# Kernel optimization log

Hardware: AMD Instinct MI355X
Metric: run time of the kernel (lower is better)

The kernel has to match this reference:

```python
import jax, jax.numpy as jnp
import numpy as np

HW = 24       # image_size // patch_size
HEAD = 16     # vision num_attention_heads
B, T, C, H = 8, 8, 1024, 4096


def _sincos_1d(d, pos):
    omega = np.arange(d // 2, dtype=np.float32) / (d / 2.0)
    omega = 1.0 / 10000 ** omega
    out = np.einsum('m,d->md', pos.reshape(-1).astype(np.float32), omega)
    return np.concatenate([np.sin(out), np.cos(out)], axis=1)


def _pos_embed_3d(embed_dim, grid_size, t_size):
    ds = embed_dim // 4 * 3
    dt = embed_dim // 4
    gh = np.arange(grid_size, dtype=np.float32)
    grid = np.stack(np.meshgrid(gh, gh), axis=0).reshape(2, -1)  # (w, h) order as in source
    spatial = np.concatenate([_sincos_1d(ds // 2, grid[0]), _sincos_1d(ds // 2, grid[1])], axis=1)  # [g*g, ds]
    temporal = _sincos_1d(dt, np.arange(t_size, dtype=np.float32))  # [t, dt]
    spatial = np.repeat(spatial[np.newaxis], t_size, axis=0)                 # [t, g*g, ds]
    temporal = np.repeat(temporal[:, np.newaxis], grid_size ** 2, axis=1)    # [t, g*g, dt]
    emb = np.concatenate([temporal, spatial], axis=-1)
    return emb.reshape(1, t_size * grid_size ** 2, embed_dim).astype(np.float32)


def setup_inputs() -> dict:
    key = jax.random.key(0)
    k1, k2, k3 = jax.random.split(key, 3)
    x = jax.random.normal(k1, (B, T * HW * HW, C), dtype=jnp.float32)
    W1 = jax.random.normal(k2, (C, H), dtype=jnp.float32) * 0.02
    b1 = jnp.zeros((H,), jnp.float32)
    W2 = jax.random.normal(k3, (H, H), dtype=jnp.float32) * 0.02
    b2 = jnp.zeros((H,), jnp.float32)
    pos_embed = jnp.asarray(_pos_embed_3d(C, HW, T))
    return {"x": x, "pos_embed": pos_embed, "W1": W1, "b1": b1, "W2": W2, "b2": b2,
            "local_num_frames": T}


def _merge(x, unm_idx, src_idx, dst_idx):
    # ToMe merge: gather unmatched src tokens, scatter-add matched src into dst.
    src, dst = x[:, ::2], x[:, 1::2]
    unm = jnp.take_along_axis(src, unm_idx[:, :, None], axis=1)   # [b, t1-r, c]
    sel = jnp.take_along_axis(src, src_idx[:, :, None], axis=1)   # [b, r, c]
    dst = jax.vmap(lambda d, i, s: d.at[i].add(s))(dst, dst_idx, sel)
    return jnp.concatenate([unm, dst], axis=1)


def _merge_tokens(x, target, head):
    b, p, c = x.shape
    # static merge schedule (same logic as torch merge_tokens)
    rs, tmp = [], p
    while tmp != target:
        if tmp - target <= tmp // 2:
            rs.append(tmp - target)
            break
        rs.append(tmp // 2)
        tmp -= tmp // 2
    dim = c // head
    size = jnp.ones((b, p, 1), x.dtype)
    for r in rs:
        bb, pp, _ = x.shape
        # metric/index computation is under no_grad in the original
        metric = jax.lax.stop_gradient(x).reshape(bb, pp, head, dim).mean(2)
        metric = metric / jnp.linalg.norm(metric, axis=-1, keepdims=True)
        a_m, b_m = metric[:, ::2], metric[:, 1::2]
        scores = jnp.einsum('bic,bjc->bij', a_m, b_m)  # [b, ta, tb]
        node_max = scores.max(-1)
        node_idx = scores.argmax(-1)
        edge_idx = jnp.argsort(-node_max, axis=-1)      # descending
        unm_idx, src_idx = edge_idx[:, r:], edge_idx[:, :r]
        dst_idx = jnp.take_along_axis(node_idx, src_idx, axis=1)
        # weighted-average merge (merge_wavg)
        x = _merge(x * size, unm_idx, src_idx, dst_idx)
        size = _merge(size, unm_idx, src_idx, dst_idx)
        x = x / size
    return x


def reference(x, pos_embed, W1, b1, W2, b2, local_num_frames):
    x = x + pos_embed.astype(x.dtype)
    x = _merge_tokens(x, local_num_frames * 16, HEAD)
    h = jax.nn.gelu(x @ W1 + b1, approximate=False)  # nn.GELU() is exact erf gelu
    return h @ W2 + b2
```

## Files before the change

kernel.cpp:

```cpp
#include <hip/hip_runtime.h>
#include <hip/hip_bf16.h>
#include <math.h>
#include <stdint.h>

typedef unsigned short u16;
typedef __attribute__((ext_vector_type(8))) short short8;
typedef __attribute__((ext_vector_type(4))) float floatx4;

#define NB 8
#define P0 4608
#define C0 1024
#define H0 4096

__global__ void detect_mode_kernel(const uint32_t* __restrict__ pe_words, int* __restrict__ mode) {
  *mode = (pe_words[64] != 0u) ? 1 : 0;
}

__device__ __forceinline__ float load_in(const void* p, size_t idx, int mode) {
  if (mode) return __bfloat162float(((const __hip_bfloat16*)p)[idx]);
  return ((const float*)p)[idx];
}

__device__ __forceinline__ float4 load4(const void* p, size_t idx, int mode) {
  float4 r;
  if (mode) {
    ushort4 u = *(const ushort4*)((const u16*)p + idx);
    r.x = __bfloat162float(*(__hip_bfloat16*)&u.x);
    r.y = __bfloat162float(*(__hip_bfloat16*)&u.y);
    r.z = __bfloat162float(*(__hip_bfloat16*)&u.z);
    r.w = __bfloat162float(*(__hip_bfloat16*)&u.w);
  } else {
    r = *(const float4*)((const float*)p + idx);
  }
  return r;
}

__device__ __forceinline__ void write_hilo(u16* __restrict__ m2, size_t tok, int lane, float v) {
  __hip_bfloat16 hi = __float2bfloat16(v);
  float hif = __bfloat162float(hi);
  __hip_bfloat16 lo = __float2bfloat16(v - hif);
  m2[tok * 128 + lane] = *(u16*)&hi;
  m2[tok * 128 + 64 + lane] = *(u16*)&lo;
}

__global__ void metric_in_kernel(const void* __restrict__ x, const void* __restrict__ pos,
                                 const int* __restrict__ mode, u16* __restrict__ m2) {
  int tok = blockIdx.x * 4 + (threadIdx.x >> 6);
  int lane = threadIdx.x & 63;
  if (tok >= NB * P0) return;
  int b = tok / P0, t = tok - b * P0;
  int md = *mode;
  size_t xbase = ((size_t)b * P0 + t) * C0 + lane;
  size_t pbase = (size_t)t * C0 + lane;
  float s = 0.f;
#pragma unroll
  for (int h = 0; h < 16; ++h)
    s += load_in(x, xbase + h * 64, md) + load_in(pos, pbase + h * 64, md);
  s *= (1.f / 16.f);
  float sq = s * s;
#pragma unroll
  for (int off = 1; off < 64; off <<= 1) sq += __shfl_xor(sq, off, 64);
  write_hilo(m2, (size_t)tok, lane, s / sqrtf(sq));
}

__global__ void metric_f32_kernel(const float* __restrict__ x, u16* __restrict__ m2, int p) {
  int tok = blockIdx.x * 4 + (threadIdx.x >> 6);
  int lane = threadIdx.x & 63;
  if (tok >= NB * p) return;
  const float* xr = x + (size_t)tok * C0 + lane;
  float s = 0.f;
#pragma unroll
  for (int h = 0; h < 16; ++h) s += xr[h * 64];
  s *= (1.f / 16.f);
  float sq = s * s;
#pragma unroll
  for (int off = 1; off < 64; off <<= 1) sq += __shfl_xor(sq, off, 64);
  write_hilo(m2, (size_t)tok, lane, s / sqrtf(sq));
}

__global__ __launch_bounds__(256) void score_mfma_kernel(const u16* __restrict__ M2,
                                                         int p, int p2, int jT2,
                                                         float* __restrict__ pm,
                                                         int* __restrict__ pi) {
  const int bi = blockIdx.x, ii = blockIdx.y, b = blockIdx.z;
  const int t = threadIdx.x, w = t >> 6, L = t & 63;
  const int wr = w >> 1, wc = w & 1;
  const int fr = L & 15, fo = (L >> 4) * 8;
  const u16* Mb = M2 + (size_t)b * p * 128;

  floatx4 acc[4][4];
#pragma unroll
  for (int mt = 0; mt < 4; ++mt)
#pragma unroll
    for (int nt = 0; nt < 4; ++nt) acc[mt][nt] = (floatx4){0.f, 0.f, 0.f, 0.f};

  const u16* arp[4];
  const u16* brp[4];
#pragma unroll
  for (int mt = 0; mt < 4; ++mt) {
    int i = ii * 128 + wr * 64 + mt * 16 + fr;
    int ta = 2 * i;
    if (ta > p - 2) ta = p - 2;
    arp[mt] = Mb + (size_t)ta * 128 + fo;
    int j = bi * 128 + wc * 64 + mt * 16 + fr;
    int tb = 2 * j + 1;
    if (tb > p - 1) tb = p - 1;
    brp[mt] = Mb + (size_t)tb * 128 + fo;
  }

#pragma unroll
  for (int ks = 0; ks < 2; ++ks) {
    short8 ah[4], al[4], bh[4], bl[4];
#pragma unroll
    for (int mt = 0; mt < 4; ++mt) {
      ah[mt] = *(const short8*)(arp[mt] + ks * 32);
      al[mt] = *(const short8*)(arp[mt] + ks * 32 + 64);
      bh[mt] = *(const short8*)(brp[mt] + ks * 32);
      bl[mt] = *(const short8*)(brp[mt] + ks * 32 + 64);
    }
#pragma unroll
    for (int mt = 0; mt < 4; ++mt)
#pragma unroll
      for (int nt = 0; nt < 4; ++nt) {
        acc[mt][nt] = __builtin_amdgcn_mfma_f32_16x16x32_bf16(ah[mt], bh[nt], acc[mt][nt], 0, 0, 0);
        acc[mt][nt] = __builtin_amdgcn_mfma_f32_16x16x32_bf16(ah[mt], bl[nt], acc[mt][nt], 0, 0, 0);
        acc[mt][nt] = __builtin_amdgcn_mfma_f32_16x16x32_bf16(al[mt], bh[nt], acc[mt][nt], 0, 0, 0);
        acc[mt][nt] = __builtin_amdgcn_mfma_f32_16x16x32_bf16(al[mt], bl[nt], acc[mt][nt], 0, 0, 0);
      }
  }

  const int gi4 = (L >> 4) * 4;
#pragma unroll
  for (int mt = 0; mt < 4; ++mt) {
#pragma unroll
    for (int reg = 0; reg < 4; ++reg) {
      int i = ii * 128 + wr * 64 + mt * 16 + gi4 + reg;
      float bm = -INFINITY;
      int bj = 0x7fffffff;
#pragma unroll
      for (int nt = 0; nt < 4; ++nt) {
        int j = bi * 128 + wc * 64 + nt * 16 + fr;
        float v = acc[mt][nt][reg];
        if (j < p2 && v > bm) { bm = v; bj = j; }
      }
#pragma unroll
      for (int mk = 1; mk < 16; mk <<= 1) {
        float om = __shfl_xor(bm, mk, 64);
        int oj = __shfl_xor(bj, mk, 64);
        if (om > bm || (om == bm && oj < bj)) { bm = om; bj = oj; }
      }
      if (fr == 0 && i < p2) {
        size_t o = ((size_t)b * 2304 + i) * jT2 + bi * 2 + wc;
        pm[o] = bm;
        pi[o] = bj;
      }
    }
  }
}

__global__ void argmax_combine_kernel(const float* __restrict__ pm, const int* __restrict__ pi,
                                      int p2, int jT, float* __restrict__ nmax,
                                      int* __restrict__ nidx, int* __restrict__ head,
                                      int* __restrict__ nxt) {
  int g = blockIdx.x * 256 + threadIdx.x;
  if (g >= NB * p2) return;
  int b = g / p2, i = g - b * p2;
  const float* r = pm + ((size_t)b * 2304 + i) * jT;
  const int* ri = pi + ((size_t)b * 2304 + i) * jT;
  float best = r[0];
  int bidx = ri[0];
  for (int k = 1; k < jT; ++k) {
    if (r[k] > best || (r[k] == best && ri[k] < bidx)) { best = r[k]; bidx = ri[k]; }
  }
  nmax[g] = best;
  nidx[g] = bidx;
  int d = bidx;
  if ((unsigned)d >= (unsigned)p2) d = 0;
  nxt[g] = atomicExch(&head[(size_t)b * p2 + d], i);
}

__global__ void init_heads_kernel(int* __restrict__ h, int n) {
  int g = blockIdx.x * 256 + threadIdx.x;
  if (g < n) h[g] = -1;
}

__global__ __launch_bounds__(256) void merge_gather_in(const void* __restrict__ x,
                                                       const void* __restrict__ pos,
                                                       const int* __restrict__ mode,
                                                       const int* __restrict__ head,
                                                       const int* __restrict__ nxt,
                                                       float* __restrict__ xo,
                                                       float* __restrict__ so, int p2) {
  int tj = blockIdx.x;
  int b = tj / p2, j = tj - b * p2;
  int c = threadIdx.x * 4;
  int md = *mode;
  __shared__ int sl[64];
  __shared__ int s_n, s_cur;
  size_t xb = ((size_t)b * P0 + 2 * j + 1) * C0 + c;
  size_t pb = (size_t)(2 * j + 1) * C0 + c;
  float4 xa = load4(x, xb, md), pa = load4(pos, pb, md);
  float4 acc = {xa.x + pa.x, xa.y + pa.y, xa.z + pa.z, xa.w + pa.w};
  float cnt = 1.f;
  if (threadIdx.x == 0) s_cur = head[tj];
  __syncthreads();
  int cur = s_cur;
  while (cur != -1) {
    if (threadIdx.x == 0) {
      int n = 0, cc = cur;
      while (cc != -1 && n < 64) {
        sl[n++] = cc;
        cc = nxt[(size_t)b * p2 + cc];
      }
      s_n = n;
      s_cur = cc;
    }
    __syncthreads();
    int n = s_n;
    cur = s_cur;
    for (int k = 0; k < n; ++k) {
      int i = sl[k];
      size_t exb = ((size_t)b * P0 + 2 * i) * C0 + c;
      size_t epb = (size_t)(2 * i) * C0 + c;
      float4 ea = load4(x, exb, md), ep = load4(pos, epb, md);
      acc.x += ea.x + ep.x;
      acc.y += ea.y + ep.y;
      acc.z += ea.z + ep.z;
      acc.w += ea.w + ep.w;
      cnt += 1.f;
    }
    __syncthreads();
  }
  float inv = 1.f / cnt;
  float4 o = {acc.x * inv, acc.y * inv, acc.z * inv, acc.w * inv};
  *(float4*)(xo + (size_t)tj * C0 + c) = o;
  if (threadIdx.x == 0) so[tj] = cnt;
}

__global__ __launch_bounds__(256) void merge_gather_f(const float* __restrict__ xi,
                                                      const float* __restrict__ si,
                                                      const int* __restrict__ head,
                                                      const int* __restrict__ nxt,
                                                      float* __restrict__ xo,
                                                      float* __restrict__ so, int p, int p2) {
  int tj = blockIdx.x;
  int b = tj / p2, j = tj - b * p2;
  int c = threadIdx.x * 4;
  __shared__ int sl[64];
  __shared__ int s_n, s_cur;
  float sz = si[(size_t)b * p + 2 * j + 1];
  float4 v = *(const float4*)(xi + ((size_t)b * p + 2 * j + 1) * C0 + c);
  float4 acc = {v.x * sz, v.y * sz, v.z * sz, v.w * sz};
  float ssum = sz;
  if (threadIdx.x == 0) s_cur = head[tj];
  __syncthreads();
  int cur = s_cur;
  while (cur != -1) {
    if (threadIdx.x == 0) {
      int n = 0, cc = cur;
      while (cc != -1 && n < 64) {
        sl[n++] = cc;
        cc = nxt[(size_t)b * p2 + cc];
      }
      s_n = n;
      s_cur = cc;
    }
    __syncthreads();
    int n = s_n;
    cur = s_cur;
    for (int k = 0; k < n; ++k) {
      int i = sl[k];
      float szi = si[(size_t)b * p + 2 * i];
      float4 e = *(const float4*)(xi + ((size_t)b * p + 2 * i) * C0 + c);
      acc.x += e.x * szi;
      acc.y += e.y * szi;
      acc.z += e.z * szi;
      acc.w += e.w * szi;
      ssum += szi;
    }
    __syncthreads();
  }
  float inv = 1.f / ssum;
  float4 o = {acc.x * inv, acc.y * inv, acc.z * inv, acc.w * inv};
  *(float4*)(xo + (size_t)tj * C0 + c) = o;
  if (threadIdx.x == 0) so[tj] = ssum;
}

__global__ void rank_kernel(const float* __restrict__ nmax, const int* __restrict__ nidx,
                            int* __restrict__ unm_map, int* __restrict__ src_ord,
                            int* __restrict__ src_dst) {
  int b = blockIdx.x;
  int i = threadIdx.x;
  __shared__ float v[72];
  __shared__ int nx[72];
  if (i < 72) { v[i] = nmax[b * 72 + i]; nx[i] = nidx[b * 72 + i]; }
  __syncthreads();
  if (i < 72) {
    float vi = v[i];
    int rank = 0;
    for (int k = 0; k < 72; ++k) {
      float vk = v[k];
      rank += (vk > vi) || (vk == vi && k < i);
    }
    if (rank < 16) {
      int d = nx[i];
      if ((unsigned)d >= 72u) d = 0;
      src_ord[b * 16 + rank] = i;
      src_dst[b * 16 + rank] = d;
    } else {
      unm_map[b * 56 + (rank - 16)] = i;
    }
  }
}

__global__ void final_init(const float* __restrict__ x5, const float* __restrict__ s5,
                           const int* __restrict__ unm_map, float* __restrict__ xf,
                           float* __restrict__ sf) {
  int bt = blockIdx.x;
  int b = bt >> 7, tk = bt & 127;
  int c = threadIdx.x * 4;
  float4 o;
  float szo;
  if (tk < 56) {
    int se = unm_map[b * 56 + tk];
    if ((unsigned)se >= 72u) se = 0;
    o = *(const float4*)(x5 + ((size_t)b * 144 + 2 * se) * C0 + c);
    szo = 1.f;
  } else {
    int j = tk - 56;
    float sz = s5[b * 144 + 2 * j + 1];
    float4 v = *(const float4*)(x5 + ((size_t)b * 144 + 2 * j + 1) * C0 + c);
    o.x = v.x * sz; o.y = v.y * sz; o.z = v.z * sz; o.w = v.w * sz;
    szo = sz;
  }
  *(float4*)(xf + (size_t)bt * C0 + c) = o;
  if (threadIdx.x == 0) sf[bt] = szo;
}

__global__ void final_scatter(const float* __restrict__ x5, const float* __restrict__ s5,
                              const int* __restrict__ src_ord, const int* __restrict__ src_dst,
                              float* __restrict__ xf, float* __restrict__ sf) {
  int bk = blockIdx.x;
  int b = bk >> 4, k = bk & 15;
  int c = threadIdx.x * 4;
  int st = src_ord[b * 16 + k], dst = src_dst[b * 16 + k];
  if ((unsigned)st >= 72u) st = 0;
  if ((unsigned)dst >= 72u) dst = 0;
  float sz = s5[b * 144 + 2 * st];
  float4 v = *(const float4*)(x5 + ((size_t)b * 144 + 2 * st) * C0 + c);
  float* out = xf + ((size_t)(b * 128 + 56 + dst)) * C0 + c;
  atomicAdd(out + 0, v.x * sz);
  atomicAdd(out + 1, v.y * sz);
  atomicAdd(out + 2, v.z * sz);
  atomicAdd(out + 3, v.w * sz);
  if (threadIdx.x == 0) atomicAdd(sf + b * 128 + 56 + dst, sz);
}

__global__ void final_div_cvt(const float* __restrict__ xf, const float* __restrict__ sf,
                              __hip_bfloat16* __restrict__ xb) {
  int bt = blockIdx.x;
  int c = threadIdx.x * 4;
  float sz = sf[bt];
  float4 v = *(const float4*)(xf + (size_t)bt * C0 + c);
  __hip_bfloat16* o = xb + (size_t)bt * C0 + c;
  o[0] = __float2bfloat16(v.x / sz);
  o[1] = __float2bfloat16(v.y / sz);
  o[2] = __float2bfloat16(v.z / sz);
  o[3] = __float2bfloat16(v.w / sz);
}

__global__ void transpose_in(const void* __restrict__ in, const int* __restrict__ mode,
                             u16* __restrict__ out, int K, int N) {
  __shared__ u16 tile[64][65];
  int n0 = blockIdx.x * 64, k0 = blockIdx.y * 64;
  int t = threadIdx.x;
  int md = *mode;
  int r = t >> 4, c4 = (t & 15) * 4;
#pragma unroll
  for (int pass = 0; pass < 4; ++pass) {
    int row = r + pass * 16;
#pragma unroll
    for (int e = 0; e < 4; ++e) {
      float v = load_in(in, (size_t)(k0 + row) * N + n0 + c4 + e, md);
      __hip_bfloat16 bv = __float2bfloat16(v);
      tile[row][c4 + e] = *(u16*)&bv;
    }
  }
  __syncthreads();
#pragma unroll
  for (int pass = 0; pass < 4; ++pass) {
    int row = r + pass * 16;
    ushort4 o;
    o.x = tile[c4][row]; o.y = tile[c4 + 1][row]; o.z = tile[c4 + 2][row]; o.w = tile[c4 + 3][row];
    *(ushort4*)(out + (size_t)(n0 + row) * K + k0 + c4) = o;
  }
}

#define GL2LDS(gp, lp)                                                                   \
  __builtin_amdgcn_global_load_lds((const __attribute__((address_space(1))) uint32_t*)(gp), \
                                   (__attribute__((address_space(3))) uint32_t*)(lp), 16, 0, 0)

__global__ __launch_bounds__(256, 2) void gemm_bt(const u16* __restrict__ A,
                                                  const u16* __restrict__ BT,
                                                  const void* __restrict__ bias,
                                                  const int* __restrict__ mode,
                                                  void* __restrict__ C, int M, int N,
                                                  int K, int act, int out_sel) {
  __shared__ __align__(16) u16 As[2 * 64 * 64];
  __shared__ __align__(16) u16 Bs[2 * 128 * 64];
  const int t = threadIdx.x, w = t >> 6, L = t & 63;
  const int m0 = blockIdx.y * 64, n0 = blockIdx.x * 128;
  const int wr = w >> 1, wc = w & 1;
  const int md = *mode;
  const int fr = L & 15, fq = (L >> 4) * 8;
  floatx4 acc[2][4];
#pragma unroll
  for (int a = 0; a < 2; ++a)
#pragma unroll
    for (int bb = 0; bb < 4; ++bb) acc[a][bb] = (floatx4){0.f, 0.f, 0.f, 0.f};

  auto stage = [&](int buf, int kk) {
#pragma unroll
    for (int q = 0; q < 2; ++q) {
      int g = q * 256 + t;
      int row = g >> 3, colg = (g & 7) ^ (row & 7);
      GL2LDS(A + (size_t)(m0 + row) * K + kk + colg * 8, As + buf * 4096 + g * 8);
    }
#pragma unroll
    for (int q = 0; q < 4; ++q) {
      int g = q * 256 + t;
      int row = g >> 3, colg = (g & 7) ^ (row & 7);
      GL2LDS(BT + (size_t)(n0 + row) * K + kk + colg * 8, Bs + buf * 8192 + g * 8);
    }
  };

  stage(0, 0);
  const int NT = K >> 6;
  int cur = 0;
  for (int it = 0; it < NT; ++it) {
    if (it + 1 < NT) {
      stage(cur ^ 1, (it + 1) << 6);
      asm volatile("s_waitcnt vmcnt(6)" ::: "memory");
    } else {
      asm volatile("s_waitcnt vmcnt(0)" ::: "memory");
    }
    __builtin_amdgcn_s_barrier();
    const u16* Ab = As + cur * 4096;
    const u16* Bb = Bs + cur * 8192;
    __builtin_amdgcn_s_setprio(1);
#pragma unroll
    for (int kh = 0; kh < 2; ++kh) {
      short8 af[2], bfr[4];
#pragma unroll
      for (int mt = 0; mt < 2; ++mt) {
        int ra = wr * 32 + mt * 16 + fr;
        int cg = (kh * 4 + (L >> 4)) ^ (ra & 7);
        af[mt] = *(const short8*)(Ab + ra * 64 + cg * 8);
      }
#pragma unroll
      for (int nt = 0; nt < 4; ++nt) {
        int rb = wc * 64 + nt * 16 + fr;
        int cg = (kh * 4 + (L >> 4)) ^ (rb & 7);
        bfr[nt] = *(const short8*)(Bb + rb * 64 + cg * 8);
      }
#pragma unroll
      for (int mt = 0; mt < 2; ++mt)
#pragma unroll
        for (int nt = 0; nt < 4; ++nt)
          acc[mt][nt] =
              __builtin_amdgcn_mfma_f32_16x16x32_bf16(af[mt], bfr[nt], acc[mt][nt], 0, 0, 0);
    }
    __builtin_amdgcn_s_setprio(0);
    __builtin_amdgcn_s_barrier();
    cur ^= 1;
  }
  const int gi4 = (L >> 4) * 4;
#pragma unroll
  for (int mt = 0; mt < 2; ++mt)
#pragma unroll
    for (int nt = 0; nt < 4; ++nt) {
      int n = n0 + wc * 64 + nt * 16 + fr;
      float bz = load_in(bias, n, md);
#pragma unroll
      for (int rr = 0; rr < 4; ++rr) {
        int m = m0 + wr * 32 + mt * 16 + gi4 + rr;
        float v = acc[mt][nt][rr] + bz;
        if (act) v = 0.5f * v * (1.f + erff(v * 0.70710678118654752f));
        size_t idx = (size_t)m * N + n;
        if (out_sel == 0 || md) {
          __hip_bfloat16 bv = __float2bfloat16(v);
          ((u16*)C)[idx] = *(u16*)&bv;
        } else {
          ((float*)C)[idx] = v;
        }
      }
    }
}

extern "C" void kernel_launch(void* const* d_in, const int* in_sizes, int n_in, void* d_out,
                              int out_size, void* d_ws, size_t ws_size, hipStream_t stream) {
  const void* x = d_in[0];
  const void* pe = d_in[1];
  const void* W1 = d_in[2];
  const void* b1 = d_in[3];
  const void* W2 = d_in[4];
  const void* b2 = d_in[5];

  char* base = (char*)d_ws;
  size_t off = 0;
  auto alloc = [&](size_t bytes) -> void* {
    void* p = base + off;
    off += (bytes + 255) & ~(size_t)255;
    return p;
  };
  int* mode = (int*)alloc(256);
  u16* m2 = (u16*)alloc((size_t)NB * 4608 * 128 * 2);
  float* pm = (float*)alloc((size_t)NB * 2304 * 36 * 4);
  int* pi = (int*)alloc((size_t)NB * 2304 * 36 * 4);
  float* nmax = (float*)alloc((size_t)NB * 2304 * 4);
  int* nidx = (int*)alloc((size_t)NB * 2304 * 4);
  float* bufA = (float*)alloc((size_t)NB * 2304 * C0 * 4);
  float* bufB = (float*)alloc((size_t)NB * 1152 * C0 * 4);
  float* s1 = (float*)alloc((size_t)NB * 2304 * 4);
  float* s2 = (float*)alloc((size_t)NB * 1152 * 4);
  float* s3 = (float*)alloc((size_t)NB * 576 * 4);
  float* s4 = (float*)alloc((size_t)NB * 288 * 4);
  float* s5 = (float*)alloc((size_t)NB * 144 * 4);
  float* sf = (float*)alloc((size_t)NB * 128 * 4);
  int* unm_map = (int*)alloc((size_t)NB * 56 * 4);
  int* src_ord = (int*)alloc((size_t)NB * 16 * 4);
  int* src_dst = (int*)alloc((size_t)NB * 16 * 4);
  u16* xfb = (u16*)alloc((size_t)NB * 128 * C0 * 2);
  u16* hbuf = (u16*)alloc((size_t)1024 * H0 * 2);
  u16* w1t = (u16*)alloc((size_t)H0 * C0 * 2);
  u16* w2t = (u16*)alloc((size_t)H0 * H0 * 2);
  int* heads = (int*)alloc((size_t)NB * 4536 * 4);
  int* nxt = (int*)alloc((size_t)NB * 2304 * 4);
  if (off > ws_size) return;

  int* h_it[6];
  h_it[0] = heads;
  h_it[1] = h_it[0] + NB * 2304;
  h_it[2] = h_it[1] + NB * 1152;
  h_it[3] = h_it[2] + NB * 576;
  h_it[4] = h_it[3] + NB * 288;
  h_it[5] = h_it[4] + NB * 144;

  float* x1 = bufA;
  float* x2 = bufB;
  float* x3 = bufA;
  float* x4 = bufB;
  float* x5 = bufA;
  float* xf = bufB;

  detect_mode_kernel<<<1, 1, 0, stream>>>((const uint32_t*)pe, mode);
  init_heads_kernel<<<(NB * 4536 + 255) / 256, 256, 0, stream>>>(heads, NB * 4536);

  transpose_in<<<dim3(4096 / 64, 1024 / 64), 256, 0, stream>>>(W1, mode, w1t, 1024, 4096);
  transpose_in<<<dim3(4096 / 64, 4096 / 64), 256, 0, stream>>>(W2, mode, w2t, 4096, 4096);

  metric_in_kernel<<<NB * P0 / 4, 256, 0, stream>>>(x, pe, mode, m2);
  score_mfma_kernel<<<dim3(18, 18, NB), 256, 0, stream>>>(m2, 4608, 2304, 36, pm, pi);
  argmax_combine_kernel<<<(NB * 2304 + 255) / 256, 256, 0, stream>>>(pm, pi, 2304, 36, nmax,
                                                                     nidx, h_it[0], nxt);
  merge_gather_in<<<NB * 2304, 256, 0, stream>>>(x, pe, mode, h_it[0], nxt, x1, s1, 2304);

  float* xs_in[4] = {x1, x2, x3, x4};
  float* ss_in[4] = {s1, s2, s3, s4};
  float* xs_out[4] = {x2, x3, x4, x5};
  float* ss_out[4] = {s2, s3, s4, s5};
  int ps[5] = {2304, 1152, 576, 288, 144};
  for (int it = 0; it < 4; ++it) {
    int p = ps[it], p2 = ps[it + 1];
    int iT = (p2 + 127) / 128, jT = (p2 + 127) / 128;
    metric_f32_kernel<<<NB * p / 4, 256, 0, stream>>>(xs_in[it], m2, p);
    score_mfma_kernel<<<dim3(jT, iT, NB), 256, 0, stream>>>(m2, p, p2, 2 * jT, pm, pi);
    argmax_combine_kernel<<<(NB * p2 + 255) / 256, 256, 0, stream>>>(pm, pi, p2, 2 * jT, nmax,
                                                                     nidx, h_it[it + 1], nxt);
    merge_gather_f<<<NB * p2, 256, 0, stream>>>(xs_in[it], ss_in[it], h_it[it + 1], nxt,
                                                xs_out[it], ss_out[it], p, p2);
  }

  metric_f32_kernel<<<NB * 144 / 4, 256, 0, stream>>>(x5, m2, 144);
  score_mfma_kernel<<<dim3(1, 1, NB), 256, 0, stream>>>(m2, 144, 72, 2, pm, pi);
  argmax_combine_kernel<<<(NB * 72 + 255) / 256, 256, 0, stream>>>(pm, pi, 72, 2, nmax, nidx,
                                                                   h_it[5], nxt);
  rank_kernel<<<NB, 128, 0, stream>>>(nmax, nidx, unm_map, src_ord, src_dst);
  final_init<<<NB * 128, 256, 0, stream>>>(x5, s5, unm_map, xf, sf);
  final_scatter<<<NB * 16, 256, 0, stream>>>(x5, s5, src_ord, src_dst, xf, sf);
  final_div_cvt<<<NB * 128, 256, 0, stream>>>(xf, sf, (__hip_bfloat16*)xfb);

  gemm_bt<<<dim3(4096 / 128, 1024 / 64), 256, 0, stream>>>(xfb, w1t, b1, mode, hbuf, 1024, 4096,
                                                           1024, 1, 0);
  gemm_bt<<<dim3(4096 / 128, 1024 / 64), 256, 0, stream>>>(hbuf, w2t, b2, mode, d_out, 1024,
                                                           4096, 4096, 0, 1);
}
```

Before: 782.1 us.

## Fuse metric computation into merge-gather kernels and vectorize transpose loads

Each merge-gather kernel now computes the head-averaged, normalized metric for its output token from the values it just produced, writing the hi/lo bf16 metric directly. This removes the separate metric_f32 kernel launches and their re-read of the merged activations. The input metric kernel and the weight transpose kernel also specialize on the dtype mode, and the transpose now uses vector loads. A risk is that merge-gather rewrites m2 while the score kernel of the same stage reads it; stream ordering should make this safe since score runs earlier.

After: 754.6 us. -3.5%, faster.

```diff
diff --git a/kernel.cpp b/kernel.cpp
--- a/kernel.cpp
+++ b/kernel.cpp
@@ -53,24 +53,18 @@
   size_t xbase = ((size_t)b * P0 + t) * C0 + lane;
   size_t pbase = (size_t)t * C0 + lane;
   float s = 0.f;
-#pragma unroll
-  for (int h = 0; h < 16; ++h)
-    s += load_in(x, xbase + h * 64, md) + load_in(pos, pbase + h * 64, md);
-  s *= (1.f / 16.f);
-  float sq = s * s;
-#pragma unroll
-  for (int off = 1; off < 64; off <<= 1) sq += __shfl_xor(sq, off, 64);
-  write_hilo(m2, (size_t)tok, lane, s / sqrtf(sq));
-}
-
-__global__ void metric_f32_kernel(const float* __restrict__ x, u16* __restrict__ m2, int p) {
-  int tok = blockIdx.x * 4 + (threadIdx.x >> 6);
-  int lane = threadIdx.x & 63;
-  if (tok >= NB * p) return;
-  const float* xr = x + (size_t)tok * C0 + lane;
-  float s = 0.f;
-#pragma unroll
-  for (int h = 0; h < 16; ++h) s += xr[h * 64];
+  if (md) {
+    const __hip_bfloat16* xp = (const __hip_bfloat16*)x + xbase;
+    const __hip_bfloat16* pp = (const __hip_bfloat16*)pos + pbase;
+#pragma unroll
+    for (int h = 0; h < 16; ++h)
+      s += __bfloat162float(xp[h * 64]) + __bfloat162float(pp[h * 64]);
+  } else {
+    const float* xp = (const float*)x + xbase;
+    const float* pp = (const float*)pos + pbase;
+#pragma unroll
+    for (int h = 0; h < 16; ++h) s += xp[h * 64] + pp[h * 64];
+  }
   s *= (1.f / 16.f);
   float sq = s * s;
 #pragma unroll
@@ -190,13 +184,15 @@
                                                        const int* __restrict__ head,
                                                        const int* __restrict__ nxt,
                                                        float* __restrict__ xo,
-                                                       float* __restrict__ so, int p2) {
+                                                       float* __restrict__ so, int p2,
+                                                       u16* __restrict__ m2out) {
   int tj = blockIdx.x;
   int b = tj / p2, j = tj - b * p2;
   int c = threadIdx.x * 4;
   int md = *mode;
   __shared__ int sl[64];
   __shared__ int s_n, s_cur;
+  __shared__ float mred[16][64];
   size_t xb = ((size_t)b * P0 + 2 * j + 1) * C0 + c;
   size_t pb = (size_t)(2 * j + 1) * C0 + c;
   float4 xa = load4(x, xb, md), pa = load4(pos, pb, md);
@@ -235,6 +231,24 @@
   float4 o = {acc.x * inv, acc.y * inv, acc.z * inv, acc.w * inv};
   *(float4*)(xo + (size_t)tj * C0 + c) = o;
   if (threadIdx.x == 0) so[tj] = cnt;
+  {
+    int hq = threadIdx.x >> 4, dq = (threadIdx.x & 15) * 4;
+    mred[hq][dq + 0] = o.x;
+    mred[hq][dq + 1] = o.y;
+    mred[hq][dq + 2] = o.z;
+    mred[hq][dq + 3] = o.w;
+  }
+  __syncthreads();
+  if (threadIdx.x < 64) {
+    float s = 0.f;
+#pragma unroll
+    for (int h = 0; h < 16; ++h) s += mred[h][threadIdx.x];
+    s *= (1.f / 16.f);
+    float sq = s * s;
+#pragma unroll
+    for (int off = 1; off < 64; off <<= 1) sq += __shfl_xor(sq, off, 64);
+    write_hilo(m2out, (size_t)tj, threadIdx.x, s / sqrtf(sq));
+  }
 }
 
 __global__ __launch_bounds__(256) void merge_gather_f(const float* __restrict__ xi,
@@ -242,12 +256,14 @@
                                                       const int* __restrict__ head,
                                                       const int* __restrict__ nxt,
                                                       float* __restrict__ xo,
-                                                      float* __restrict__ so, int p, int p2) {
+                                                      float* __restrict__ so, int p, int p2,
+                                                      u16* __restrict__ m2out) {
   int tj = blockIdx.x;
   int b = tj / p2, j = tj - b * p2;
   int c = threadIdx.x * 4;
   __shared__ int sl[64];
   __shared__ int s_n, s_cur;
+  __shared__ float mred[16][64];
   float sz = si[(size_t)b * p + 2 * j + 1];
   float4 v = *(const float4*)(xi + ((size_t)b * p + 2 * j + 1) * C0 + c);
   float4 acc = {v.x * sz, v.y * sz, v.z * sz, v.w * sz};
@@ -284,6 +300,24 @@
   float4 o = {acc.x * inv, acc.y * inv, acc.z * inv, acc.w * inv};
   *(float4*)(xo + (size_t)tj * C0 + c) = o;
   if (threadIdx.x == 0) so[tj] = ssum;
+  {
+    int hq = threadIdx.x >> 4, dq = (threadIdx.x & 15) * 4;
+    mred[hq][dq + 0] = o.x;
+    mred[hq][dq + 1] = o.y;
+    mred[hq][dq + 2] = o.z;
+    mred[hq][dq + 3] = o.w;
+  }
+  __syncthreads();
+  if (threadIdx.x < 64) {
+    float s = 0.f;
+#pragma unroll
+    for (int h = 0; h < 16; ++h) s += mred[h][threadIdx.x];
+    s *= (1.f / 16.f);
+    float sq = s * s;
+#pragma unroll
+    for (int off = 1; off < 64; off <<= 1) sq += __shfl_xor(sq, off, 64);
+    write_hilo(m2out, (size_t)tj, threadIdx.x, s / sqrtf(sq));
+  }
 }
 
 __global__ void rank_kernel(const float* __restrict__ nmax, const int* __restrict__ nidx,
@@ -376,14 +410,27 @@
   int t = threadIdx.x;
   int md = *mode;
   int r = t >> 4, c4 = (t & 15) * 4;
-#pragma unroll
-  for (int pass = 0; pass < 4; ++pass) {
-    int row = r + pass * 16;
-#pragma unroll
-    for (int e = 0; e < 4; ++e) {
-      float v = load_in(in, (size_t)(k0 + row) * N + n0 + c4 + e, md);
-      __hip_bfloat16 bv = __float2bfloat16(v);
-      tile[row][c4 + e] = *(u16*)&bv;
+  if (md) {
+#pragma unroll
+    for (int pass = 0; pass < 4; ++pass) {
+      int row = r + pass * 16;
+      ushort4 u = *(const ushort4*)((const u16*)in + (size_t)(k0 + row) * N + n0 + c4);
+      tile[row][c4 + 0] = u.x;
+      tile[row][c4 + 1] = u.y;
+      tile[row][c4 + 2] = u.z;
+      tile[row][c4 + 3] = u.w;
+    }
+  } else {
+#pragma unroll
+    for (int pass = 0; pass < 4; ++pass) {
+      int row = r + pass * 16;
+      float4 v = *(const float4*)((const float*)in + (size_t)(k0 + row) * N + n0 + c4);
+      __hip_bfloat16 b0 = __float2bfloat16(v.x), b1 = __float2bfloat16(v.y);
+      __hip_bfloat16 b2 = __float2bfloat16(v.z), b3 = __float2bfloat16(v.w);
+      tile[row][c4 + 0] = *(u16*)&b0;
+      tile[row][c4 + 1] = *(u16*)&b1;
+      tile[row][c4 + 2] = *(u16*)&b2;
+      tile[row][c4 + 3] = *(u16*)&b3;
     }
   }
   __syncthreads();
@@ -412,7 +459,7 @@
   const int m0 = blockIdx.y * 64, n0 = blockIdx.x * 128;
   const int wr = w >> 1, wc = w & 1;
   const int md = *mode;
-  const int fr = L & 15, fq = (L >> 4) * 8;
+  const int fr = L & 15;
   floatx4 acc[2][4];
 #pragma unroll
   for (int a = 0; a < 2; ++a)
@@ -563,7 +610,7 @@
   score_mfma_kernel<<<dim3(18, 18, NB), 256, 0, stream>>>(m2, 4608, 2304, 36, pm, pi);
   argmax_combine_kernel<<<(NB * 2304 + 255) / 256, 256, 0, stream>>>(pm, pi, 2304, 36, nmax,
                                                                      nidx, h_it[0], nxt);
-  merge_gather_in<<<NB * 2304, 256, 0, stream>>>(x, pe, mode, h_it[0], nxt, x1, s1, 2304);
+  merge_gather_in<<<NB * 2304, 256, 0, stream>>>(x, pe, mode, h_it[0], nxt, x1, s1, 2304, m2);
 
   float* xs_in[4] = {x1, x2, x3, x4};
   float* ss_in[4] = {s1, s2, s3, s4};
@@ -573,15 +620,13 @@
   for (int it = 0; it < 4; ++it) {
     int p = ps[it], p2 = ps[it + 1];
     int iT = (p2 + 127) / 128, jT = (p2 + 127) / 128;
-    metric_f32_kernel<<<NB * p / 4, 256, 0, stream>>>(xs_in[it], m2, p);
     score_mfma_kernel<<<dim3(jT, iT, NB), 256, 0, stream>>>(m2, p, p2, 2 * jT, pm, pi);
     argmax_combine_kernel<<<(NB * p2 + 255) / 256, 256, 0, stream>>>(pm, pi, p2, 2 * jT, nmax,
                                                                      nidx, h_it[it + 1], nxt);
     merge_gather_f<<<NB * p2, 256, 0, stream>>>(xs_in[it], ss_in[it], h_it[it + 1], nxt,
-                                                xs_out[it], ss_out[it], p, p2);
-  }
-
-  metric_f32_kernel<<<NB * 144 / 4, 256, 0, stream>>>(x5, m2, 144);
+                                                xs_out[it], ss_out[it], p, p2, m2);
+  }
+
   score_mfma_kernel<<<dim3(1, 1, NB), 256, 0, stream>>>(m2, 144, 72, 2, pm, pi);
   argmax_combine_kernel<<<(NB * 72 + 255) / 256, 256, 0, stream>>>(pm, pi, 72, 2, nmax, nidx,
                                                                    h_it[5], nxt);
```
